# Performance work log

Hardware: AMD Instinct MI355X
Metric: run time of the kernel (lower is better)

Reference implementation:

```python
import jax, jax.numpy as jnp
import numpy as np

N_Q = 16
N_K = 16
D_QK = 64
D_V = 64
# torch module default scale=1.0 saturates softmax at feature width 1024;
# we use the conventional sqrt(d) scale for well-conditioned numerics.
SCALE = 32.0  # sqrt(N_Q * D_QK)
DROPOUT_P = 0.0  # dropout is identity at p=0


def setup_inputs() -> dict:
    key = jax.random.key(0)
    kq, kk, kv = jax.random.split(key, 3)
    S = 8192
    return {
        "query": jax.random.normal(kq, (S, N_Q, D_QK), dtype=jnp.float32),
        "key": jax.random.normal(kk, (S, N_K, D_QK), dtype=jnp.float32),
        "value": jax.random.normal(kv, (S, N_K, D_V), dtype=jnp.float32),
    }


def reference(query, key, value):
    # Flatten trailing (head, dim) into one feature axis, as the torch view does.
    q = query.reshape(-1, N_Q * D_QK)            # [S_q, 1024]
    k = key.reshape(-1, N_K * D_QK)              # [S_k, 1024]
    v = value.reshape(-1, N_K * D_V)             # [S_k, 1024]
    scores = jnp.matmul(q, k.T) / SCALE          # [S_q, S_k]
    attn = jax.nn.softmax(scores, axis=-1)       # dropout_p=0 -> identity
    out = jnp.matmul(attn, v)                    # [S_q, 1024]
    return out.reshape(query.shape[:-1] + (-1,))  # [S_q, N_Q, D_V]
```

## Files before the change

### kernel.cpp

```cpp
#include <hip/hip_runtime.h>
#include <hip/hip_bf16.h>


typedef __bf16 bf16x8 __attribute__((ext_vector_type(8)));
typedef float f32x4 __attribute__((ext_vector_type(4)));
typedef const __attribute__((address_space(1))) unsigned int* as1p;
typedef __attribute__((address_space(3))) unsigned int* as3p;
typedef unsigned short u16;

__device__ __forceinline__ u16 f2bf(float x) {
  unsigned u = __float_as_uint(x);
  u += 0x7fffu + ((u >> 16) & 1u);
  return (u16)(u >> 16);
}
__device__ __forceinline__ float bf2f(u16 b) { return __uint_as_float(((unsigned)b) << 16); }
__device__ __forceinline__ unsigned pack2(float lo, float hi) {
  return (unsigned)f2bf(lo) | ((unsigned)f2bf(hi) << 16);
}

#define BAR() __builtin_amdgcn_s_barrier()
#define LGKM0() do { asm volatile("s_waitcnt lgkmcnt(0)" ::: "memory"); __builtin_amdgcn_sched_barrier(0); } while (0)
#define VMC0()  do { asm volatile("s_waitcnt vmcnt(0)"  ::: "memory"); __builtin_amdgcn_sched_barrier(0); } while (0)

__global__ __launch_bounds__(256) void cvt_bf16(const float* __restrict__ in,
                                                unsigned short* __restrict__ out) {
  const size_t i = (size_t)blockIdx.x * 256 + threadIdx.x;
  const float4* p = (const float4*)in + i * 2;
  float4 a = p[0], b = p[1];
  uint4 o;
  o.x = pack2(a.x, a.y);
  o.y = pack2(a.z, a.w);
  o.z = pack2(b.x, b.y);
  o.w = pack2(b.z, b.w);
  ((uint4*)out)[i] = o;
}

__global__ __launch_bounds__(256) void transpose_bf16(const float* __restrict__ V,
                                                      unsigned short* __restrict__ VT) {
  __shared__ float t[64][65];
  const int rb = blockIdx.x * 64;
  const int cb = blockIdx.y * 64;
  const int tid = threadIdx.x;
#pragma unroll
  for (int it = 0; it < 4; ++it) {
    int r = it * 16 + (tid >> 4);
    int c = (tid & 15) * 4;
    float4 x = *(const float4*)(V + (size_t)(rb + r) * 1024 + cb + c);
    t[r][c] = x.x; t[r][c + 1] = x.y; t[r][c + 2] = x.z; t[r][c + 3] = x.w;
  }
  __syncthreads();
  const int j = tid & 63;
  const int c0 = (tid >> 6) * 16;
#pragma unroll
  for (int i = 0; i < 16; ++i) {
    int c = c0 + i;
    VT[(size_t)(cb + c) * 8192 + rb + j] = f2bf(t[j][c]);
  }
}

template <int BN, int OUTMODE>
__global__ __launch_bounds__(512, 2) void gemm8p(const u16* __restrict__ A,
                                                 const u16* __restrict__ B,
                                                 void* __restrict__ Cv,
                                                 const float* __restrict__ inv,
                                                 int K, int ldc, int ntn, float scale) {
  constexpr int NF = BN / 64;
  constexpr int ABUF = 32768;
  constexpr int BBUF = BN * 128;
  constexpr int NBJ = BN / 64;
  __shared__ __align__(1024) char smem[2 * ABUF + 2 * BBUF];
  char* Alds = smem;
  char* Blds = smem + 2 * ABUF;

  const int tid = threadIdx.x;
  const int lane = tid & 63, wave = tid >> 6;
  const int wr = wave >> 2, wc = wave & 3;
  const int lan15 = lane & 15, g = lane >> 4, l7 = lane & 7;

  const int nwg = gridDim.x;
  const int wg = (blockIdx.x & 7) * (nwg >> 3) + (blockIdx.x >> 3);
  const int bm0 = (wg / ntn) * 256;
  const int bn0 = (wg % ntn) * BN;

  const int sr = tid >> 3;
  const int scb = ((tid & 7) ^ (sr & 7)) * 8;
  const u16* Ag = A + (size_t)(bm0 + sr) * K + scb;
  const u16* Bg = B + (size_t)(bn0 + sr) * K + scb;
  const int sdst = wave * 1024;

  const int sa0 = ((g) ^ l7) * 16;
  const int sa1 = ((4 + g) ^ l7) * 16;
  const int arow = (wr * 128 + lan15) * 128;
  const int brow = (wc * (BN / 4) + lan15) * 128;

  f32x4 acc[8][NF];
#pragma unroll
  for (int m = 0; m < 8; ++m)
#pragma unroll
    for (int n = 0; n < NF; ++n) acc[m][n] = f32x4{0.f, 0.f, 0.f, 0.f};

  const int nt = K >> 6;

#pragma unroll
  for (int j = 0; j < 4; ++j)
    __builtin_amdgcn_global_load_lds((as1p)(Ag + (size_t)j * 64 * K),
                                     (as3p)(Alds + j * 8192 + sdst), 16, 0, 0);
#pragma unroll
  for (int j = 0; j < NBJ; ++j)
    __builtin_amdgcn_global_load_lds((as1p)(Bg + (size_t)j * 64 * K),
                                     (as3p)(Blds + j * 8192 + sdst), 16, 0, 0);
  VMC0();
  BAR();

  bf16x8 a[4][2], bfr[NF][2];

  for (int t = 0; t < nt; ++t) {
    const int buf = t & 1;
    const int nbuf = buf ^ 1;
    const char* Ab = Alds + buf * ABUF;
    const char* Bb = Blds + buf * BBUF;
    const size_t koff = (size_t)(t + 1) * 64;
    const bool pf = (t + 1 < nt);

    if constexpr (BN == 256) {
#pragma unroll
      for (int m = 0; m < 4; ++m) {
        a[m][0] = *(const bf16x8*)(Ab + arow + m * 2048 + sa0);
        a[m][1] = *(const bf16x8*)(Ab + arow + m * 2048 + sa1);
      }
#pragma unroll
      for (int n = 0; n < 4; ++n) {
        bfr[n][0] = *(const bf16x8*)(Bb + brow + n * 2048 + sa0);
        bfr[n][1] = *(const bf16x8*)(Bb + brow + n * 2048 + sa1);
      }
      if (pf) {
#pragma unroll
        for (int j = 0; j < 4; ++j)
          __builtin_amdgcn_global_load_lds((as1p)(Ag + (size_t)j * 64 * K + koff),
                                           (as3p)(Alds + nbuf * ABUF + j * 8192 + sdst), 16, 0, 0);
      }
      BAR(); LGKM0();
      __builtin_amdgcn_s_setprio(1);
#pragma unroll
      for (int m = 0; m < 4; ++m)
#pragma unroll
        for (int n = 0; n < 2; ++n)
#pragma unroll
          for (int ks = 0; ks < 2; ++ks)
            acc[m][n] = __builtin_amdgcn_mfma_f32_16x16x32_bf16(a[m][ks], bfr[n][ks], acc[m][n], 0, 0, 0);
      __builtin_amdgcn_s_setprio(0);
      BAR();

      if (pf) {
#pragma unroll
        for (int j = 0; j < NBJ; ++j)
          __builtin_amdgcn_global_load_lds((as1p)(Bg + (size_t)j * 64 * K + koff),
                                           (as3p)(Blds + nbuf * BBUF + j * 8192 + sdst), 16, 0, 0);
      }
      BAR();
      __builtin_amdgcn_s_setprio(1);
#pragma unroll
      for (int m = 0; m < 4; ++m)
#pragma unroll
        for (int n = 0; n < 2; ++n)
#pragma unroll
          for (int ks = 0; ks < 2; ++ks)
            acc[m][2 + n] = __builtin_amdgcn_mfma_f32_16x16x32_bf16(a[m][ks], bfr[2 + n][ks], acc[m][2 + n], 0, 0, 0);
      __builtin_amdgcn_s_setprio(0);
      BAR();

#pragma unroll
      for (int m = 0; m < 4; ++m) {
        a[m][0] = *(const bf16x8*)(Ab + arow + 8192 + m * 2048 + sa0);
        a[m][1] = *(const bf16x8*)(Ab + arow + 8192 + m * 2048 + sa1);
      }
      BAR(); LGKM0();
      __builtin_amdgcn_s_setprio(1);
#pragma unroll
      for (int m = 0; m < 4; ++m)
#pragma unroll
        for (int n = 0; n < 2; ++n)
#pragma unroll
          for (int ks = 0; ks < 2; ++ks)
            acc[4 + m][n] = __builtin_amdgcn_mfma_f32_16x16x32_bf16(a[m][ks], bfr[n][ks], acc[4 + m][n], 0, 0, 0);
      __builtin_amdgcn_s_setprio(0);
      BAR();

      VMC0();
      BAR();
      __builtin_amdgcn_s_setprio(1);
#pragma unroll
      for (int m = 0; m < 4; ++m)
#pragma unroll
        for (int n = 0; n < 2; ++n)
#pragma unroll
          for (int ks = 0; ks < 2; ++ks)
            acc[4 + m][2 + n] = __builtin_amdgcn_mfma_f32_16x16x32_bf16(a[m][ks], bfr[2 + n][ks], acc[4 + m][2 + n], 0, 0, 0);
      __builtin_amdgcn_s_setprio(0);
      BAR();
    } else {
#pragma unroll
      for (int m = 0; m < 4; ++m) {
        a[m][0] = *(const bf16x8*)(Ab + arow + m * 2048 + sa0);
        a[m][1] = *(const bf16x8*)(Ab + arow + m * 2048 + sa1);
      }
#pragma unroll
      for (int n = 0; n < 2; ++n) {
        bfr[n][0] = *(const bf16x8*)(Bb + brow + n * 2048 + sa0);
        bfr[n][1] = *(const bf16x8*)(Bb + brow + n * 2048 + sa1);
      }
      if (pf) {
#pragma unroll
        for (int j = 0; j < 4; ++j)
          __builtin_amdgcn_global_load_lds((as1p)(Ag + (size_t)j * 64 * K + koff),
                                           (as3p)(Alds + nbuf * ABUF + j * 8192 + sdst), 16, 0, 0);
#pragma unroll
        for (int j = 0; j < NBJ; ++j)
          __builtin_amdgcn_global_load_lds((as1p)(Bg + (size_t)j * 64 * K + koff),
                                           (as3p)(Blds + nbuf * BBUF + j * 8192 + sdst), 16, 0, 0);
      }
      BAR(); LGKM0();
      __builtin_amdgcn_s_setprio(1);
#pragma unroll
      for (int m = 0; m < 4; ++m)
#pragma unroll
        for (int n = 0; n < 2; ++n)
#pragma unroll
          for (int ks = 0; ks < 2; ++ks)
            acc[m][n] = __builtin_amdgcn_mfma_f32_16x16x32_bf16(a[m][ks], bfr[n][ks], acc[m][n], 0, 0, 0);
      __builtin_amdgcn_s_setprio(0);
      BAR();

#pragma unroll
      for (int m = 0; m < 4; ++m) {
        a[m][0] = *(const bf16x8*)(Ab + arow + 8192 + m * 2048 + sa0);
        a[m][1] = *(const bf16x8*)(Ab + arow + 8192 + m * 2048 + sa1);
      }
      VMC0();
      BAR(); LGKM0();
      __builtin_amdgcn_s_setprio(1);
#pragma unroll
      for (int m = 0; m < 4; ++m)
#pragma unroll
        for (int n = 0; n < 2; ++n)
#pragma unroll
          for (int ks = 0; ks < 2; ++ks)
            acc[4 + m][n] = __builtin_amdgcn_mfma_f32_16x16x32_bf16(a[m][ks], bfr[n][ks], acc[4 + m][n], 0, 0, 0);
      __builtin_amdgcn_s_setprio(0);
      BAR();
    }
  }

  const int r0 = bm0 + wr * 128 + g * 4;
  const int c0 = bn0 + wc * (BN / 4) + lan15;
  if constexpr (OUTMODE == 0) {
    u16* C = (u16*)Cv;
#pragma unroll
    for (int m = 0; m < 8; ++m)
#pragma unroll
      for (int n = 0; n < NF; ++n)
#pragma unroll
        for (int r = 0; r < 4; ++r)
          C[(size_t)(r0 + m * 16 + r) * ldc + c0 + n * 16] = f2bf(__expf(acc[m][n][r] * scale));
  } else {
    float* C = (float*)Cv;
#pragma unroll
    for (int m = 0; m < 8; ++m)
#pragma unroll
      for (int r = 0; r < 4; ++r) {
        const int row = r0 + m * 16 + r;
        const float iv = inv ? inv[row] : 1.0f;
#pragma unroll
        for (int n = 0; n < NF; ++n)
          C[(size_t)row * ldc + c0 + n * 16] = acc[m][n][r] * iv;
      }
  }
}

__global__ __launch_bounds__(256) void rowsum_inv(const u16* __restrict__ E,
                                                  float* __restrict__ inv) {
  __shared__ float red[4];
  const u16* row = E + (size_t)blockIdx.x * 8192;
  const int tid = threadIdx.x;
  float s = 0.f;
#pragma unroll
  for (int c = 0; c < 4; ++c) {
    uint4 v = *((const uint4*)row + c * 256 + tid);
    unsigned u[4] = {v.x, v.y, v.z, v.w};
#pragma unroll
    for (int q = 0; q < 4; ++q)
      s += bf2f((u16)(u[q] & 0xffffu)) + bf2f((u16)(u[q] >> 16));
  }
#pragma unroll
  for (int off = 32; off; off >>= 1) s += __shfl_xor(s, off, 64);
  if ((tid & 63) == 0) red[tid >> 6] = s;
  __syncthreads();
  if (tid == 0) inv[blockIdx.x] = 1.0f / ((red[0] + red[1]) + (red[2] + red[3]));
}

__global__ __launch_bounds__(256) void normalize_inplace(u16* __restrict__ E) {
  __shared__ float red[4];
  u16* row = E + (size_t)blockIdx.x * 8192;
  const int tid = threadIdx.x;
  uint4 v[4];
  float f[32];
  float s = 0.f;
#pragma unroll
  for (int c = 0; c < 4; ++c) {
    v[c] = *((const uint4*)row + c * 256 + tid);
    unsigned u[4] = {v[c].x, v[c].y, v[c].z, v[c].w};
#pragma unroll
    for (int q = 0; q < 4; ++q) {
      f[c * 8 + q * 2] = bf2f((u16)(u[q] & 0xffffu));
      f[c * 8 + q * 2 + 1] = bf2f((u16)(u[q] >> 16));
      s += f[c * 8 + q * 2] + f[c * 8 + q * 2 + 1];
    }
  }
#pragma unroll
  for (int off = 32; off; off >>= 1) s += __shfl_xor(s, off, 64);
  if ((tid & 63) == 0) red[tid >> 6] = s;
  __syncthreads();
  const float iv = 1.0f / ((red[0] + red[1]) + (red[2] + red[3]));
#pragma unroll
  for (int c = 0; c < 4; ++c) {
    uint4 o;
    o.x = pack2(f[c * 8 + 0] * iv, f[c * 8 + 1] * iv);
    o.y = pack2(f[c * 8 + 2] * iv, f[c * 8 + 3] * iv);
    o.z = pack2(f[c * 8 + 4] * iv, f[c * 8 + 5] * iv);
    o.w = pack2(f[c * 8 + 6] * iv, f[c * 8 + 7] * iv);
    *((uint4*)row + c * 256 + tid) = o;
  }
}

extern "C" void kernel_launch(void* const* d_in, const int* in_sizes, int n_in,
                              void* d_out, int out_size, void* d_ws, size_t ws_size,
                              hipStream_t stream) {
  const float* Q = (const float*)d_in[0];
  const float* K = (const float*)d_in[1];
  const float* V = (const float*)d_in[2];

  char* ws = (char*)d_ws;
  u16* S = (u16*)ws;
  u16* VT = (u16*)(ws + (size_t)134217728);
  float* invsum = (float*)(ws + (size_t)134217728 + 16777216);
  const bool haveInv = ws_size >= (size_t)134217728 + 16777216 + 32768;

  u16* Qb = (u16*)d_out;
  u16* Kb = Qb + 8388608;

  cvt_bf16<<<4096, 256, 0, stream>>>(Q, Qb);
  cvt_bf16<<<4096, 256, 0, stream>>>(K, Kb);
  transpose_bf16<<<dim3(128, 16), 256, 0, stream>>>(V, VT);

  gemm8p<256, 0><<<1024, 512, 0, stream>>>(Qb, Kb, S, nullptr, 1024, 8192, 32, 1.0f / 32.0f);

  if (haveInv) {
    rowsum_inv<<<8192, 256, 0, stream>>>(S, invsum);
    gemm8p<128, 1><<<256, 512, 0, stream>>>(S, VT, d_out, invsum, 8192, 1024, 8, 1.0f);
  } else {
    normalize_inplace<<<8192, 256, 0, stream>>>(S);
    gemm8p<128, 1><<<256, 512, 0, stream>>>(S, VT, d_out, nullptr, 8192, 1024, 8, 1.0f);
  }
}
```

Measured before the change: 331.7 us.

## Replace GEMM with ring-buffered pipeline and fuse row-sum partials into exp epilogue

Replaces the double-buffered GEMM with a generic ring-buffer kernel whose prefetch depth is configurable (3 stages for the attn·V GEMM, using partial vmcnt waits). The second GEMM's tiles become 128x256 instead of 256x128. The score GEMM epilogue now emits per-row partial sums of the exponentials, so a tiny rowinv kernel can replace the rowsum pass that re-read the full 128MB bf16 score matrix. This trades an extra partials buffer and shuffle reductions in the epilogue for removing a large memory pass and improving load/compute overlap.

```diff
diff --git a/kernel.cpp b/kernel.cpp
--- a/kernel.cpp
+++ b/kernel.cpp
@@ -18,9 +18,8 @@
   return (unsigned)f2bf(lo) | ((unsigned)f2bf(hi) << 16);
 }
 
-#define BAR() __builtin_amdgcn_s_barrier()
+#define BAR()   do { __builtin_amdgcn_s_barrier(); __builtin_amdgcn_sched_barrier(0); } while (0)
 #define LGKM0() do { asm volatile("s_waitcnt lgkmcnt(0)" ::: "memory"); __builtin_amdgcn_sched_barrier(0); } while (0)
-#define VMC0()  do { asm volatile("s_waitcnt vmcnt(0)"  ::: "memory"); __builtin_amdgcn_sched_barrier(0); } while (0)
 
 __global__ __launch_bounds__(256) void cvt_bf16(const float* __restrict__ in,
                                                 unsigned short* __restrict__ out) {
@@ -58,19 +57,22 @@
   }
 }
 
-template <int BN, int OUTMODE>
-__global__ __launch_bounds__(512, 2) void gemm8p(const u16* __restrict__ A,
-                                                 const u16* __restrict__ B,
-                                                 void* __restrict__ Cv,
-                                                 const float* __restrict__ inv,
-                                                 int K, int ldc, int ntn, float scale) {
-  constexpr int NF = BN / 64;
-  constexpr int ABUF = 32768;
-  constexpr int BBUF = BN * 128;
-  constexpr int NBJ = BN / 64;
-  __shared__ __align__(1024) char smem[2 * ABUF + 2 * BBUF];
-  char* Alds = smem;
-  char* Blds = smem + 2 * ABUF;
+template <int BM, int DEPTH, int OUTMODE>
+__global__ __launch_bounds__(512, 2) void gemm_ring(const u16* __restrict__ A,
+                                                    const u16* __restrict__ B,
+                                                    void* __restrict__ Cv,
+                                                    const float* __restrict__ inv,
+                                                    float* __restrict__ partials,
+                                                    int K, int ldc, int ntn, float scale) {
+  constexpr int MF = BM / 32;
+  constexpr int LA = BM / 64;
+  constexpr int LB = 4;
+  constexpr int ABUF = BM * 128;
+  constexpr int BBUF = 256 * 128;
+  constexpr int BUFSZ = ABUF + BBUF;
+  constexpr int LPT = LA + LB;
+
+  __shared__ __align__(1024) char smem[DEPTH * BUFSZ];
 
   const int tid = threadIdx.x;
   const int lane = tid & 63, wave = tid >> 6;
@@ -79,236 +81,173 @@
 
   const int nwg = gridDim.x;
   const int wg = (blockIdx.x & 7) * (nwg >> 3) + (blockIdx.x >> 3);
-  const int bm0 = (wg / ntn) * 256;
-  const int bn0 = (wg % ntn) * BN;
+  const int bm0 = (wg / ntn) * BM;
+  const int bn0 = (wg % ntn) * 256;
 
   const int sr = tid >> 3;
   const int scb = ((tid & 7) ^ (sr & 7)) * 8;
-  const u16* Ag = A + (size_t)(bm0 + sr) * K + scb;
-  const u16* Bg = B + (size_t)(bn0 + sr) * K + scb;
-  const int sdst = wave * 1024;
-
-  const int sa0 = ((g) ^ l7) * 16;
+  const u16* Ags = A + (size_t)(bm0 + sr) * K + scb;
+  const u16* Bgs = B + (size_t)(bn0 + sr) * K + scb;
+
+  const int sa0 = ((0 + g) ^ l7) * 16;
   const int sa1 = ((4 + g) ^ l7) * 16;
-  const int arow = (wr * 128 + lan15) * 128;
-  const int brow = (wc * (BN / 4) + lan15) * 128;
-
-  f32x4 acc[8][NF];
-#pragma unroll
-  for (int m = 0; m < 8; ++m)
-#pragma unroll
-    for (int n = 0; n < NF; ++n) acc[m][n] = f32x4{0.f, 0.f, 0.f, 0.f};
+  const int abase = (wr * (BM / 2) + lan15) * 128;
+  const int bbase = ABUF + (wc * 64 + lan15) * 128;
+
+  f32x4 acc[MF][4];
+#pragma unroll
+  for (int m = 0; m < MF; ++m)
+#pragma unroll
+    for (int n = 0; n < 4; ++n) acc[m][n] = f32x4{0.f, 0.f, 0.f, 0.f};
 
   const int nt = K >> 6;
 
-#pragma unroll
-  for (int j = 0; j < 4; ++j)
-    __builtin_amdgcn_global_load_lds((as1p)(Ag + (size_t)j * 64 * K),
-                                     (as3p)(Alds + j * 8192 + sdst), 16, 0, 0);
-#pragma unroll
-  for (int j = 0; j < NBJ; ++j)
-    __builtin_amdgcn_global_load_lds((as1p)(Bg + (size_t)j * 64 * K),
-                                     (as3p)(Blds + j * 8192 + sdst), 16, 0, 0);
-  VMC0();
-  BAR();
-
-  bf16x8 a[4][2], bfr[NF][2];
+  auto ISSUE = [&](int t, int off) {
+    const size_t ko = (size_t)t * 64;
+#pragma unroll
+    for (int j = 0; j < LA; ++j)
+      __builtin_amdgcn_global_load_lds((as1p)(Ags + (size_t)j * 64 * K + ko),
+                                       (as3p)(smem + off + j * 8192 + tid * 16), 16, 0, 0);
+#pragma unroll
+    for (int j = 0; j < LB; ++j)
+      __builtin_amdgcn_global_load_lds((as1p)(Bgs + (size_t)j * 64 * K + ko),
+                                       (as3p)(smem + off + ABUF + j * 8192 + tid * 16), 16, 0, 0);
+  };
+
+#pragma unroll
+  for (int p = 0; p < DEPTH - 1; ++p)
+    if (p < nt) ISSUE(p, p * BUFSZ);
+
+  int cbuf = 0;
+  int ibuf = (DEPTH - 1) * BUFSZ;
+  if (ibuf >= DEPTH * BUFSZ) ibuf -= DEPTH * BUFSZ;
+
+  bf16x8 af[4][2], bf[4][2];
 
   for (int t = 0; t < nt; ++t) {
-    const int buf = t & 1;
-    const int nbuf = buf ^ 1;
-    const char* Ab = Alds + buf * ABUF;
-    const char* Bb = Blds + buf * BBUF;
-    const size_t koff = (size_t)(t + 1) * 64;
-    const bool pf = (t + 1 < nt);
-
-    if constexpr (BN == 256) {
-#pragma unroll
-      for (int m = 0; m < 4; ++m) {
-        a[m][0] = *(const bf16x8*)(Ab + arow + m * 2048 + sa0);
-        a[m][1] = *(const bf16x8*)(Ab + arow + m * 2048 + sa1);
+    if (t + DEPTH - 2 < nt) {
+      if constexpr (DEPTH == 3) asm volatile("s_waitcnt vmcnt(6)" ::: "memory");
+      else                      asm volatile("s_waitcnt vmcnt(0)" ::: "memory");
+    } else {
+      asm volatile("s_waitcnt vmcnt(0)" ::: "memory");
+    }
+    __builtin_amdgcn_sched_barrier(0);
+    BAR();
+
+    if (t + DEPTH - 1 < nt) ISSUE(t + DEPTH - 1, ibuf);
+
+    if constexpr (MF == 8) {
+#pragma unroll
+      for (int mh = 0; mh < 2; ++mh) {
+#pragma unroll
+        for (int m = 0; m < 4; ++m) {
+          af[m][0] = *(const bf16x8*)(smem + cbuf + abase + (mh * 4 + m) * 2048 + sa0);
+          af[m][1] = *(const bf16x8*)(smem + cbuf + abase + (mh * 4 + m) * 2048 + sa1);
+        }
+        if (mh == 0) {
+#pragma unroll
+          for (int n = 0; n < 4; ++n) {
+            bf[n][0] = *(const bf16x8*)(smem + cbuf + bbase + n * 2048 + sa0);
+            bf[n][1] = *(const bf16x8*)(smem + cbuf + bbase + n * 2048 + sa1);
+          }
+        }
+        LGKM0();
+        __builtin_amdgcn_s_setprio(1);
+#pragma unroll
+        for (int m = 0; m < 4; ++m)
+#pragma unroll
+          for (int n = 0; n < 4; ++n)
+#pragma unroll
+            for (int ks = 0; ks < 2; ++ks)
+              acc[mh * 4 + m][n] =
+                  __builtin_amdgcn_mfma_f32_16x16x32_bf16(af[m][ks], bf[n][ks], acc[mh * 4 + m][n], 0, 0, 0);
+        __builtin_amdgcn_s_setprio(0);
       }
-#pragma unroll
-      for (int n = 0; n < 4; ++n) {
-        bfr[n][0] = *(const bf16x8*)(Bb + brow + n * 2048 + sa0);
-        bfr[n][1] = *(const bf16x8*)(Bb + brow + n * 2048 + sa1);
+    } else {
+#pragma unroll
+      for (int ks = 0; ks < 2; ++ks) {
+        const int sa = (ks == 0) ? sa0 : sa1;
+#pragma unroll
+        for (int m = 0; m < 4; ++m)
+          af[m][ks] = *(const bf16x8*)(smem + cbuf + abase + m * 2048 + sa);
+#pragma unroll
+        for (int n = 0; n < 4; ++n)
+          bf[n][ks] = *(const bf16x8*)(smem + cbuf + bbase + n * 2048 + sa);
+        LGKM0();
+        __builtin_amdgcn_s_setprio(1);
+#pragma unroll
+        for (int m = 0; m < 4; ++m)
+#pragma unroll
+          for (int n = 0; n < 4; ++n)
+            acc[m][n] = __builtin_amdgcn_mfma_f32_16x16x32_bf16(af[m][ks], bf[n][ks], acc[m][n], 0, 0, 0);
+        __builtin_amdgcn_s_setprio(0);
       }
-      if (pf) {
-#pragma unroll
-        for (int j = 0; j < 4; ++j)
-          __builtin_amdgcn_global_load_lds((as1p)(Ag + (size_t)j * 64 * K + koff),
-                                           (as3p)(Alds + nbuf * ABUF + j * 8192 + sdst), 16, 0, 0);
-      }
-      BAR(); LGKM0();
-      __builtin_amdgcn_s_setprio(1);
-#pragma unroll
-      for (int m = 0; m < 4; ++m)
-#pragma unroll
-        for (int n = 0; n < 2; ++n)
-#pragma unroll
-          for (int ks = 0; ks < 2; ++ks)
-            acc[m][n] = __builtin_amdgcn_mfma_f32_16x16x32_bf16(a[m][ks], bfr[n][ks], acc[m][n], 0, 0, 0);
-      __builtin_amdgcn_s_setprio(0);
-      BAR();
-
-      if (pf) {
-#pragma unroll
-        for (int j = 0; j < NBJ; ++j)
-          __builtin_amdgcn_global_load_lds((as1p)(Bg + (size_t)j * 64 * K + koff),
-                                           (as3p)(Blds + nbuf * BBUF + j * 8192 + sdst), 16, 0, 0);
-      }
-      BAR();
-      __builtin_amdgcn_s_setprio(1);
-#pragma unroll
-      for (int m = 0; m < 4; ++m)
-#pragma unroll
-        for (int n = 0; n < 2; ++n)
-#pragma unroll
-          for (int ks = 0; ks < 2; ++ks)
-            acc[m][2 + n] = __builtin_amdgcn_mfma_f32_16x16x32_bf16(a[m][ks], bfr[2 + n][ks], acc[m][2 + n], 0, 0, 0);
-      __builtin_amdgcn_s_setprio(0);
-      BAR();
-
-#pragma unroll
-      for (int m = 0; m < 4; ++m) {
-        a[m][0] = *(const bf16x8*)(Ab + arow + 8192 + m * 2048 + sa0);
-        a[m][1] = *(const bf16x8*)(Ab + arow + 8192 + m * 2048 + sa1);
-      }
-      BAR(); LGKM0();
-      __builtin_amdgcn_s_setprio(1);
-#pragma unroll
-      for (int m = 0; m < 4; ++m)
-#pragma unroll
-        for (int n = 0; n < 2; ++n)
-#pragma unroll
-          for (int ks = 0; ks < 2; ++ks)
-            acc[4 + m][n] = __builtin_amdgcn_mfma_f32_16x16x32_bf16(a[m][ks], bfr[n][ks], acc[4 + m][n], 0, 0, 0);
-      __builtin_amdgcn_s_setprio(0);
-      BAR();
-
-      VMC0();
-      BAR();
-      __builtin_amdgcn_s_setprio(1);
-#pragma unroll
-      for (int m = 0; m < 4; ++m)
-#pragma unroll
-        for (int n = 0; n < 2; ++n)
-#pragma unroll
-          for (int ks = 0; ks < 2; ++ks)
-            acc[4 + m][2 + n] = __builtin_amdgcn_mfma_f32_16x16x32_bf16(a[m][ks], bfr[2 + n][ks], acc[4 + m][2 + n], 0, 0, 0);
-      __builtin_amdgcn_s_setprio(0);
-      BAR();
-    } else {
-#pragma unroll
-      for (int m = 0; m < 4; ++m) {
-        a[m][0] = *(const bf16x8*)(Ab + arow + m * 2048 + sa0);
-        a[m][1] = *(const bf16x8*)(Ab + arow + m * 2048 + sa1);
-      }
-#pragma unroll
-      for (int n = 0; n < 2; ++n) {
-        bfr[n][0] = *(const bf16x8*)(Bb + brow + n * 2048 + sa0);
-        bfr[n][1] = *(const bf16x8*)(Bb + brow + n * 2048 + sa1);
-      }
-      if (pf) {
-#pragma unroll
-        for (int j = 0; j < 4; ++j)
-          __builtin_amdgcn_global_load_lds((as1p)(Ag + (size_t)j * 64 * K + koff),
-                                           (as3p)(Alds + nbuf * ABUF + j * 8192 + sdst), 16, 0, 0);
-#pragma unroll
-        for (int j = 0; j < NBJ; ++j)
-          __builtin_amdgcn_global_load_lds((as1p)(Bg + (size_t)j * 64 * K + koff),
-                                           (as3p)(Blds + nbuf * BBUF + j * 8192 + sdst), 16, 0, 0);
-      }
-      BAR(); LGKM0();
-      __builtin_amdgcn_s_setprio(1);
-#pragma unroll
-      for (int m = 0; m < 4; ++m)
-#pragma unroll
-        for (int n = 0; n < 2; ++n)
-#pragma unroll
-          for (int ks = 0; ks < 2; ++ks)
-            acc[m][n] = __builtin_amdgcn_mfma_f32_16x16x32_bf16(a[m][ks], bfr[n][ks], acc[m][n], 0, 0, 0);
-      __builtin_amdgcn_s_setprio(0);
-      BAR();
-
-#pragma unroll
-      for (int m = 0; m < 4; ++m) {
-        a[m][0] = *(const bf16x8*)(Ab + arow + 8192 + m * 2048 + sa0);
-        a[m][1] = *(const bf16x8*)(Ab + arow + 8192 + m * 2048 + sa1);
-      }
-      VMC0();
-      BAR(); LGKM0();
-      __builtin_amdgcn_s_setprio(1);
-#pragma unroll
-      for (int m = 0; m < 4; ++m)
-#pragma unroll
-        for (int n = 0; n < 2; ++n)
-#pragma unroll
-          for (int ks = 0; ks < 2; ++ks)
-            acc[4 + m][n] = __builtin_amdgcn_mfma_f32_16x16x32_bf16(a[m][ks], bfr[n][ks], acc[4 + m][n], 0, 0, 0);
-      __builtin_amdgcn_s_setprio(0);
-      BAR();
     }
-  }
-
-  const int r0 = bm0 + wr * 128 + g * 4;
-  const int c0 = bn0 + wc * (BN / 4) + lan15;
+
+    cbuf += BUFSZ; if (cbuf == DEPTH * BUFSZ) cbuf = 0;
+    ibuf += BUFSZ; if (ibuf == DEPTH * BUFSZ) ibuf = 0;
+  }
+
+  const int c0 = bn0 + wc * 64 + lan15;
   if constexpr (OUTMODE == 0) {
     u16* C = (u16*)Cv;
-#pragma unroll
-    for (int m = 0; m < 8; ++m)
-#pragma unroll
-      for (int n = 0; n < NF; ++n)
-#pragma unroll
-        for (int r = 0; r < 4; ++r)
-          C[(size_t)(r0 + m * 16 + r) * ldc + c0 + n * 16] = f2bf(__expf(acc[m][n][r] * scale));
+    const int cb4 = (bn0 >> 8) * 4 + wc;
+#pragma unroll
+    for (int m = 0; m < MF; ++m)
+#pragma unroll
+      for (int r = 0; r < 4; ++r) {
+        const int row = bm0 + wr * (BM / 2) + m * 16 + g * 4 + r;
+        float part = 0.f;
+#pragma unroll
+        for (int n = 0; n < 4; ++n) {
+          float v = __expf(acc[m][n][r] * scale);
+          C[(size_t)row * ldc + c0 + n * 16] = f2bf(v);
+          part += v;
+        }
+        part += __shfl_xor(part, 1, 64);
+        part += __shfl_xor(part, 2, 64);
+        part += __shfl_xor(part, 4, 64);
+        part += __shfl_xor(part, 8, 64);
+        if (lan15 == 0) partials[(size_t)row * 128 + cb4] = part;
+      }
   } else {
     float* C = (float*)Cv;
 #pragma unroll
-    for (int m = 0; m < 8; ++m)
+    for (int m = 0; m < MF; ++m)
 #pragma unroll
       for (int r = 0; r < 4; ++r) {
-        const int row = r0 + m * 16 + r;
+        const int row = bm0 + wr * (BM / 2) + m * 16 + g * 4 + r;
         const float iv = inv ? inv[row] : 1.0f;
 #pragma unroll
-        for (int n = 0; n < NF; ++n)
+        for (int n = 0; n < 4; ++n)
           C[(size_t)row * ldc + c0 + n * 16] = acc[m][n][r] * iv;
       }
   }
 }
 
-__global__ __launch_bounds__(256) void rowsum_inv(const u16* __restrict__ E,
-                                                  float* __restrict__ inv) {
-  __shared__ float red[4];
-  const u16* row = E + (size_t)blockIdx.x * 8192;
-  const int tid = threadIdx.x;
+__global__ __launch_bounds__(256) void rowinv(const float* __restrict__ partials,
+                                              float* __restrict__ inv) {
+  const int row = blockIdx.x * 256 + threadIdx.x;
+  const float4* p = (const float4*)(partials + (size_t)row * 128);
   float s = 0.f;
 #pragma unroll
-  for (int c = 0; c < 4; ++c) {
-    uint4 v = *((const uint4*)row + c * 256 + tid);
-    unsigned u[4] = {v.x, v.y, v.z, v.w};
-#pragma unroll
-    for (int q = 0; q < 4; ++q)
-      s += bf2f((u16)(u[q] & 0xffffu)) + bf2f((u16)(u[q] >> 16));
-  }
-#pragma unroll
-  for (int off = 32; off; off >>= 1) s += __shfl_xor(s, off, 64);
-  if ((tid & 63) == 0) red[tid >> 6] = s;
-  __syncthreads();
-  if (tid == 0) inv[blockIdx.x] = 1.0f / ((red[0] + red[1]) + (red[2] + red[3]));
+  for (int j = 0; j < 32; ++j) {
+    float4 v = p[j];
+    s += (v.x + v.y) + (v.z + v.w);
+  }
+  inv[row] = 1.0f / s;
 }
 
 __global__ __launch_bounds__(256) void normalize_inplace(u16* __restrict__ E) {
   __shared__ float red[4];
   u16* row = E + (size_t)blockIdx.x * 8192;
   const int tid = threadIdx.x;
-  uint4 v[4];
   float f[32];
   float s = 0.f;
 #pragma unroll
   for (int c = 0; c < 4; ++c) {
-    v[c] = *((const uint4*)row + c * 256 + tid);
-    unsigned u[4] = {v[c].x, v[c].y, v[c].z, v[c].w};
+    uint4 v = *((const uint4*)row + c * 256 + tid);
+    unsigned u[4] = {v.x, v.y, v.z, v.w};
 #pragma unroll
     for (int q = 0; q < 4; ++q) {
       f[c * 8 + q * 2] = bf2f((u16)(u[q] & 0xffffu));
@@ -342,8 +281,10 @@
   char* ws = (char*)d_ws;
   u16* S = (u16*)ws;
   u16* VT = (u16*)(ws + (size_t)134217728);
-  float* invsum = (float*)(ws + (size_t)134217728 + 16777216);
-  const bool haveInv = ws_size >= (size_t)134217728 + 16777216 + 32768;
+  float* partials = (float*)(ws + (size_t)134217728 + 16777216);
+  float* inv = (float*)(ws + (size_t)134217728 + 16777216 + 4194304);
+  const bool haveInv =
+      ws_size >= (size_t)134217728 + 16777216 + 4194304 + 32768;
 
   u16* Qb = (u16*)d_out;
   u16* Kb = Qb + 8388608;
@@ -352,13 +293,17 @@
   cvt_bf16<<<4096, 256, 0, stream>>>(K, Kb);
   transpose_bf16<<<dim3(128, 16), 256, 0, stream>>>(V, VT);
 
-  gemm8p<256, 0><<<1024, 512, 0, stream>>>(Qb, Kb, S, nullptr, 1024, 8192, 32, 1.0f / 32.0f);
+  gemm_ring<256, 2, 0><<<1024, 512, 0, stream>>>(
+      Qb, Kb, S, nullptr, haveInv ? partials : (float*)(ws + 134217728 + 16777216),
+      1024, 8192, 32, 1.0f / 32.0f);
 
   if (haveInv) {
-    rowsum_inv<<<8192, 256, 0, stream>>>(S, invsum);
-    gemm8p<128, 1><<<256, 512, 0, stream>>>(S, VT, d_out, invsum, 8192, 1024, 8, 1.0f);
+    rowinv<<<32, 256, 0, stream>>>(partials, inv);
+    gemm_ring<128, 3, 1><<<256, 512, 0, stream>>>(
+        S, VT, d_out, inv, nullptr, 8192, 1024, 4, 1.0f);
   } else {
     normalize_inplace<<<8192, 256, 0, stream>>>(S);
-    gemm8p<128, 1><<<256, 512, 0, stream>>>(S, VT, d_out, nullptr, 8192, 1024, 8, 1.0f);
-  }
-}
+    gemm_ring<128, 3, 1><<<256, 512, 0, stream>>>(
+        S, VT, d_out, nullptr, nullptr, 8192, 1024, 4, 1.0f);
+  }
+}
```

Result: faster. 313.1 us (-5.6%).
